# Optimization experiments

Hardware: AMD Instinct MI355X
Metric: run time of the kernel (lower is better)

Reference implementation:

```python
import jax, jax.numpy as jnp
import numpy as np

NUM_LEVELS = 16
MIN_RES = 16
MAX_RES = 4096
LOG2_HASHMAP_SIZE = 19
FEATURES_PER_LEVEL = 2
TABLE_SIZE = 1 << LOG2_HASHMAP_SIZE
HASH_INIT_SCALE = 0.001
N_POINTS = 1 << 20

_growth = np.exp((np.log(MAX_RES) - np.log(MIN_RES)) / (NUM_LEVELS - 1))
SCALINGS = jnp.asarray(np.floor(MIN_RES * _growth ** np.arange(NUM_LEVELS)), dtype=jnp.float32)  # [L]
HASH_OFFSET = jnp.arange(NUM_LEVELS, dtype=jnp.int32) * TABLE_SIZE  # [L]
PRIMES = jnp.array([1, 2654435761, 805459861], dtype=jnp.uint32)
# corner selection (1 -> ceil, 0 -> floor) matching hashed_0..hashed_7 in the torch code
CORNER_MASK = jnp.array([[1,1,1],[1,0,1],[0,0,1],[0,1,1],[1,1,0],[1,0,0],[0,0,0],[0,1,0]], dtype=bool)


def _hash(coords):
    # coords: int32 [..., L, 3]. torch uses int64 products, but since TABLE_SIZE
    # is a power of two dividing 2^32, uint32 wraparound is bit-identical mod TABLE_SIZE.
    u = coords.astype(jnp.uint32) * PRIMES
    h = u[..., 0] ^ u[..., 1] ^ u[..., 2]
    h = h & jnp.uint32(TABLE_SIZE - 1)
    return h.astype(jnp.int32) + HASH_OFFSET  # [..., L]


def setup_inputs() -> dict:
    key = jax.random.key(0)
    kx, kt = jax.random.split(key)
    x = jax.random.uniform(kx, (N_POINTS, 3), dtype=jnp.float32)
    hash_table = (jax.random.uniform(kt, (TABLE_SIZE * NUM_LEVELS, FEATURES_PER_LEVEL),
                                     dtype=jnp.float32) * 2.0 - 1.0) * HASH_INIT_SCALE
    return {"x": x, "hash_table": hash_table}


def reference(x, hash_table):
    # x: [N, 3] in [0,1]; hash_table: [TABLE_SIZE*L, F]
    scaled = x[:, None, :] * SCALINGS[None, :, None]          # [N, L, 3]
    scaled_f = jnp.floor(scaled)
    scaled_c = jnp.ceil(scaled)
    offset = scaled - scaled_f                                 # [N, L, 3]
    cf = scaled_f.astype(jnp.int32)
    cc = scaled_c.astype(jnp.int32)
    corners = jnp.where(CORNER_MASK[:, None, None, :], cc[None], cf[None])  # [8, N, L, 3]
    idx = _hash(corners)                                       # [8, N, L]
    f = hash_table[idx]                                        # [8, N, L, F]
    ox, oy, oz = offset[..., 0:1], offset[..., 1:2], offset[..., 2:3]
    f03 = f[0] * ox + f[3] * (1 - ox)
    f12 = f[1] * ox + f[2] * (1 - ox)
    f56 = f[5] * ox + f[6] * (1 - ox)
    f47 = f[4] * ox + f[7] * (1 - ox)
    f0312 = f03 * oy + f12 * (1 - oy)
    f4756 = f47 * oy + f56 * (1 - oy)
    enc = f0312 * oz + f4756 * (1 - oz)                        # [N, L, F]
    return enc.reshape(enc.shape[0], NUM_LEVELS * FEATURES_PER_LEVEL)  # [N, L*F]
```

## Files before the change

### kernel.cpp

```cpp
#include <hip/hip_runtime.h>
#include <hip/hip_fp16.h>
#include <math.h>

#define NPTS   (1u << 20)
#define NLVL   16
#define NGRID  5
#define TBITS  19
#define TMASK  ((1u << TBITS) - 1u)
#define CHUNKS (NPTS / 256u)
#define PR1    2654435761u
#define PR2    805459861u

struct Params {
    float    s[NLVL];
    uint32_t gdim[NGRID];
    uint32_t goff[NGRID];
    uint32_t vcum[NGRID + 1];
};

__device__ __forceinline__ void load_pair(const float2* __restrict__ t,
                                          uint32_t iF, uint32_t iC,
                                          float2& vF, float2& vC)
{
    const uint32_t d = iF ^ iC;
    if (d == 1u) {
        const float4 q = *(const float4*)(t + (iF & ~1u));
        if (iF & 1u) { vF = make_float2(q.z, q.w); vC = make_float2(q.x, q.y); }
        else         { vF = make_float2(q.x, q.y); vC = make_float2(q.z, q.w); }
    } else if (iC == iF + 1u || iF == iC + 1u) {
        const uint32_t lo = (iF < iC) ? iF : iC;
        const float4 q = *(const float4*)(t + lo);
        if (iF == lo) { vF = make_float2(q.x, q.y); vC = make_float2(q.z, q.w); }
        else          { vF = make_float2(q.z, q.w); vC = make_float2(q.x, q.y); }
    } else {
        vF = t[iF]; vC = t[iC];
    }
}

__device__ __forceinline__ float2 lerp8(float2 f0, float2 f1, float2 f2, float2 f3,
                                        float2 f4, float2 f5, float2 f6, float2 f7,
                                        float ox, float oy, float oz)
{
    const float omx = 1.0f - ox, omy = 1.0f - oy, omz = 1.0f - oz;
    const float a0 = f0.x * ox + f3.x * omx, b0 = f0.y * ox + f3.y * omx;
    const float a1 = f1.x * ox + f2.x * omx, b1 = f1.y * ox + f2.y * omx;
    const float a2 = f5.x * ox + f6.x * omx, b2 = f5.y * ox + f6.y * omx;
    const float a3 = f4.x * ox + f7.x * omx, b3 = f4.y * ox + f7.y * omx;
    const float c0 = a0 * oy + a1 * omy, d0 = b0 * oy + b1 * omy;
    const float c1 = a3 * oy + a2 * omy, d1 = b3 * oy + b2 * omy;
    return make_float2(c0 * oz + c1 * omz, d0 * oz + d1 * omz);
}

__device__ __forceinline__ float2 eval_hash(float x0, float x1, float x2,
                                            float s, uint32_t l,
                                            const float2* __restrict__ table)
{
    const float sx = x0 * s, sy = x1 * s, sz = x2 * s;
    const float fxf = floorf(sx), fyf = floorf(sy), fzf = floorf(sz);
    const float cxf = ceilf(sx),  cyf = ceilf(sy),  czf = ceilf(sz);
    const float ox = sx - fxf, oy = sy - fyf, oz = sz - fzf;

    const uint32_t fx = (uint32_t)fxf, cx = (uint32_t)cxf;
    const uint32_t Yf = (uint32_t)fyf * PR1,  Yc = (uint32_t)cyf * PR1;
    const uint32_t Zf = (uint32_t)fzf * PR2,  Zc = (uint32_t)czf * PR2;
    const uint32_t base = l << TBITS;

    const uint32_t i0 = ((cx ^ Yc ^ Zc) & TMASK) + base;
    const uint32_t i1 = ((cx ^ Yf ^ Zc) & TMASK) + base;
    const uint32_t i2 = ((fx ^ Yf ^ Zc) & TMASK) + base;
    const uint32_t i3 = ((fx ^ Yc ^ Zc) & TMASK) + base;
    const uint32_t i4 = ((cx ^ Yc ^ Zf) & TMASK) + base;
    const uint32_t i5 = ((cx ^ Yf ^ Zf) & TMASK) + base;
    const uint32_t i6 = ((fx ^ Yf ^ Zf) & TMASK) + base;
    const uint32_t i7 = ((fx ^ Yc ^ Zf) & TMASK) + base;

    float2 f0, f1, f2, f3, f4, f5, f6, f7;
    load_pair(table, i3, i0, f3, f0);
    load_pair(table, i2, i1, f2, f1);
    load_pair(table, i7, i4, f7, f4);
    load_pair(table, i6, i5, f6, f5);
    return lerp8(f0, f1, f2, f3, f4, f5, f6, f7, ox, oy, oz);
}

__device__ __forceinline__ float2 eval_grid(float x0, float x1, float x2,
                                            float s,
                                            const float2* __restrict__ g,
                                            uint32_t d)
{
    const float sx = x0 * s, sy = x1 * s, sz = x2 * s;
    const float fxf = floorf(sx), fyf = floorf(sy), fzf = floorf(sz);
    const float cxf = ceilf(sx),  cyf = ceilf(sy),  czf = ceilf(sz);
    const float ox = sx - fxf, oy = sy - fyf, oz = sz - fzf;

    const uint32_t fx = (uint32_t)fxf, fy = (uint32_t)fyf, fz = (uint32_t)fzf;
    const uint32_t cy = (uint32_t)cyf, cz = (uint32_t)czf;
    const bool xadj = ((uint32_t)cxf == fx + 1u);

    const uint32_t bA = (cz * d + cy) * d + fx;
    const uint32_t bB = (cz * d + fy) * d + fx;
    const uint32_t bC = (fz * d + cy) * d + fx;
    const uint32_t bD = (fz * d + fy) * d + fx;
    const float4 qA = *(const float4*)(g + bA);
    const float4 qB = *(const float4*)(g + bB);
    const float4 qC = *(const float4*)(g + bC);
    const float4 qD = *(const float4*)(g + bD);

    const float2 f3 = make_float2(qA.x, qA.y);
    const float2 f0 = xadj ? make_float2(qA.z, qA.w) : f3;
    const float2 f2 = make_float2(qB.x, qB.y);
    const float2 f1 = xadj ? make_float2(qB.z, qB.w) : f2;
    const float2 f7 = make_float2(qC.x, qC.y);
    const float2 f4 = xadj ? make_float2(qC.z, qC.w) : f7;
    const float2 f6 = make_float2(qD.x, qD.y);
    const float2 f5 = xadj ? make_float2(qD.z, qD.w) : f6;
    return lerp8(f0, f1, f2, f3, f4, f5, f6, f7, ox, oy, oz);
}

__global__ __launch_bounds__(256)
void build_grids(const float2* __restrict__ table, float2* __restrict__ gridbuf,
                 Params P)
{
    const uint32_t t = blockIdx.x * 256u + threadIdx.x;
    if (t >= P.vcum[NGRID]) return;
    uint32_t l = 0;
    #pragma unroll
    for (int i = 1; i < NGRID; ++i) if (t >= P.vcum[i]) l = i;
    const uint32_t v = t - P.vcum[l];
    const uint32_t d = P.gdim[l];
    const uint32_t vz = v / (d * d);
    const uint32_t r1 = v - vz * d * d;
    const uint32_t vy = r1 / d;
    const uint32_t vx = r1 - vy * d;
    const uint32_t h = ((vx ^ (vy * PR1) ^ (vz * PR2)) & TMASK) + (l << TBITS);
    gridbuf[P.goff[l] + v] = table[h];
}

__global__ __launch_bounds__(256)
void gather16(const float* __restrict__ x,
              const float2* __restrict__ table,
              const float2* __restrict__ gridbuf,
              __half2* __restrict__ stage,
              Params P)
{
    const uint32_t l = blockIdx.x / CHUNKS;
    const uint32_t p = (blockIdx.x % CHUNKS) * 256u + threadIdx.x;

    const float x0 = x[p * 3 + 0];
    const float x1 = x[p * 3 + 1];
    const float x2 = x[p * 3 + 2];

    float2 e;
    if (l < NGRID)
        e = eval_grid(x0, x1, x2, P.s[l], gridbuf + P.goff[l], P.gdim[l]);
    else
        e = eval_hash(x0, x1, x2, P.s[l], l, table);
    stage[l * NPTS + p] = __floats2half2_rn(e.x, e.y);
}

__global__ __launch_bounds__(256)
void transpose_kernel(const __half2* __restrict__ stage, float4* __restrict__ out4)
{
    const uint32_t e = blockIdx.x * 256u + threadIdx.x;
    const uint32_t p = e >> 3;
    const uint32_t j = e & 7u;
    const float2 a = __half22float2(stage[(2u*j)     * NPTS + p]);
    const float2 b = __half22float2(stage[(2u*j + 1) * NPTS + p]);
    out4[e] = make_float4(a.x, a.y, b.x, b.y);
}

__global__ __launch_bounds__(256)
void hashenc_fused(const float* __restrict__ x,
                   const float2* __restrict__ table,
                   float2* __restrict__ out,
                   Params P)
{
    const uint32_t tid = blockIdx.x * 256u + threadIdx.x;
    const uint32_t p = tid >> 4;
    const uint32_t l = tid & 15u;
    out[p * 16u + l] = eval_hash(x[p*3+0], x[p*3+1], x[p*3+2], P.s[l], l, table);
}

extern "C" void kernel_launch(void* const* d_in, const int* in_sizes, int n_in,
                              void* d_out, int out_size, void* d_ws, size_t ws_size,
                              hipStream_t stream) {
    const float*  x     = (const float*)d_in[0];
    const float2* table = (const float2*)d_in[1];

    Params P;
    const double growth = exp((log(4096.0) - log(16.0)) / 15.0);
    for (int l = 0; l < NLVL; ++l)
        P.s[l] = (float)floor(16.0 * pow(growth, (double)l));

    uint32_t vtot = 0;
    for (int l = 0; l < NGRID; ++l) {
        const uint32_t d = (uint32_t)P.s[l] + 1u;
        P.gdim[l] = d;
        P.vcum[l] = vtot;
        P.goff[l] = vtot;
        vtot += d * d * d;
    }
    P.vcum[NGRID] = vtot;

    const size_t grid_bytes  = (((size_t)vtot * sizeof(float2)) + 255u) & ~(size_t)255u;
    const size_t stage_bytes = (size_t)NPTS * NLVL * sizeof(__half2);
    const size_t ws_needed   = grid_bytes + stage_bytes;

    if (ws_size >= ws_needed) {
        float2*  gridbuf = (float2*)d_ws;
        __half2* stage   = (__half2*)((char*)d_ws + grid_bytes);
        float4*  out4    = (float4*)d_out;

        dim3 b256(256u);
        hipLaunchKernelGGL(build_grids, dim3((vtot + 255u) / 256u), b256, 0, stream,
                           table, gridbuf, P);
        hipLaunchKernelGGL(gather16, dim3(NLVL * CHUNKS), b256, 0, stream,
                           x, table, gridbuf, stage, P);
        hipLaunchKernelGGL(transpose_kernel, dim3(NPTS * 8u / 256u), b256, 0, stream,
                           stage, out4);
    } else {
        float2* out = (float2*)d_out;
        hipLaunchKernelGGL(hashenc_fused, dim3(NPTS * NLVL / 256u), dim3(256u), 0, stream,
                           x, table, out, P);
    }
}
```

Measured before the change: 378.7 us.

## Issue table gathers via inline asm with sc0 hint and nontemporal stage/output stores

Replaces the compiler-generated gather loads in the hash and grid evaluators with inline-asm global_load instructions carrying an sc0 cache hint. All four pair loads are issued before a single vmcnt(0) wait, so the gathers overlap. The fp16 stage writes and the final output writes become nontemporal stores to reduce cache pollution. Forcing the wait and blocking the scheduler with a sched barrier may limit compiler scheduling, and the changed cache policy could hurt reuse of the hash table.

Result: slower. 388.3 us (+2.5%).

```diff
diff --git a/kernel.cpp b/kernel.cpp
--- a/kernel.cpp
+++ b/kernel.cpp
@@ -11,6 +11,8 @@
 #define PR1    2654435761u
 #define PR2    805459861u
 
+typedef float vf4 __attribute__((ext_vector_type(4)));
+
 struct Params {
     float    s[NLVL];
     uint32_t gdim[NGRID];
@@ -18,23 +20,37 @@
     uint32_t vcum[NGRID + 1];
 };
 
-__device__ __forceinline__ void load_pair(const float2* __restrict__ t,
-                                          uint32_t iF, uint32_t iC,
-                                          float2& vF, float2& vC)
-{
-    const uint32_t d = iF ^ iC;
-    if (d == 1u) {
-        const float4 q = *(const float4*)(t + (iF & ~1u));
-        if (iF & 1u) { vF = make_float2(q.z, q.w); vC = make_float2(q.x, q.y); }
-        else         { vF = make_float2(q.x, q.y); vC = make_float2(q.z, q.w); }
-    } else if (iC == iF + 1u || iF == iC + 1u) {
-        const uint32_t lo = (iF < iC) ? iF : iC;
-        const float4 q = *(const float4*)(t + lo);
-        if (iF == lo) { vF = make_float2(q.x, q.y); vC = make_float2(q.z, q.w); }
-        else          { vF = make_float2(q.z, q.w); vC = make_float2(q.x, q.y); }
+__device__ __forceinline__ void issue_pair(const float2* __restrict__ t,
+                                           uint32_t iF, uint32_t iC,
+                                           float4& q, float2& a, float2& b,
+                                           bool& merged, bool& swp)
+{
+    const uint32_t lo = iF < iC ? iF : iC;
+    const uint32_t hi = iF < iC ? iC : iF;
+    merged = (hi - lo == 1u);
+    swp    = merged && (iF == hi);
+    if (merged) {
+        asm volatile("global_load_dwordx4 %0, %1, off sc0"
+                     : "=v"(q) : "v"(t + lo));
     } else {
-        vF = t[iF]; vC = t[iC];
-    }
+        asm volatile("global_load_dwordx2 %0, %1, off sc0"
+                     : "=v"(a) : "v"(t + iF));
+        asm volatile("global_load_dwordx2 %0, %1, off sc0"
+                     : "=v"(b) : "v"(t + iC));
+    }
+}
+
+__device__ __forceinline__ float2 sel_F(const float4& q, const float2& a,
+                                        bool merged, bool swp)
+{
+    if (merged) return swp ? make_float2(q.z, q.w) : make_float2(q.x, q.y);
+    return a;
+}
+__device__ __forceinline__ float2 sel_C(const float4& q, const float2& b,
+                                        bool merged, bool swp)
+{
+    if (merged) return swp ? make_float2(q.x, q.y) : make_float2(q.z, q.w);
+    return b;
 }
 
 __device__ __forceinline__ float2 lerp8(float2 f0, float2 f1, float2 f2, float2 f3,
@@ -74,11 +90,20 @@
     const uint32_t i6 = ((fx ^ Yf ^ Zf) & TMASK) + base;
     const uint32_t i7 = ((fx ^ Yc ^ Zf) & TMASK) + base;
 
-    float2 f0, f1, f2, f3, f4, f5, f6, f7;
-    load_pair(table, i3, i0, f3, f0);
-    load_pair(table, i2, i1, f2, f1);
-    load_pair(table, i7, i4, f7, f4);
-    load_pair(table, i6, i5, f6, f5);
+    float4 qA, qB, qC, qD;
+    float2 aA, bA, aB, bB, aC, bC, aD, bD;
+    bool mA, sA, mB, sB, mC, sC, mD, sD;
+    issue_pair(table, i3, i0, qA, aA, bA, mA, sA);
+    issue_pair(table, i2, i1, qB, aB, bB, mB, sB);
+    issue_pair(table, i7, i4, qC, aC, bC, mC, sC);
+    issue_pair(table, i6, i5, qD, aD, bD, mD, sD);
+    asm volatile("s_waitcnt vmcnt(0)" ::: "memory");
+    __builtin_amdgcn_sched_barrier(0);
+
+    const float2 f3 = sel_F(qA, aA, mA, sA), f0 = sel_C(qA, bA, mA, sA);
+    const float2 f2 = sel_F(qB, aB, mB, sB), f1 = sel_C(qB, bB, mB, sB);
+    const float2 f7 = sel_F(qC, aC, mC, sC), f4 = sel_C(qC, bC, mC, sC);
+    const float2 f6 = sel_F(qD, aD, mD, sD), f5 = sel_C(qD, bD, mD, sD);
     return lerp8(f0, f1, f2, f3, f4, f5, f6, f7, ox, oy, oz);
 }
 
@@ -100,10 +125,14 @@
     const uint32_t bB = (cz * d + fy) * d + fx;
     const uint32_t bC = (fz * d + cy) * d + fx;
     const uint32_t bD = (fz * d + fy) * d + fx;
-    const float4 qA = *(const float4*)(g + bA);
-    const float4 qB = *(const float4*)(g + bB);
-    const float4 qC = *(const float4*)(g + bC);
-    const float4 qD = *(const float4*)(g + bD);
+
+    float4 qA, qB, qC, qD;
+    asm volatile("global_load_dwordx4 %0, %1, off sc0" : "=v"(qA) : "v"(g + bA));
+    asm volatile("global_load_dwordx4 %0, %1, off sc0" : "=v"(qB) : "v"(g + bB));
+    asm volatile("global_load_dwordx4 %0, %1, off sc0" : "=v"(qC) : "v"(g + bC));
+    asm volatile("global_load_dwordx4 %0, %1, off sc0" : "=v"(qD) : "v"(g + bD));
+    asm volatile("s_waitcnt vmcnt(0)" ::: "memory");
+    __builtin_amdgcn_sched_barrier(0);
 
     const float2 f3 = make_float2(qA.x, qA.y);
     const float2 f0 = xadj ? make_float2(qA.z, qA.w) : f3;
@@ -154,18 +183,37 @@
         e = eval_grid(x0, x1, x2, P.s[l], gridbuf + P.goff[l], P.gdim[l]);
     else
         e = eval_hash(x0, x1, x2, P.s[l], l, table);
-    stage[l * NPTS + p] = __floats2half2_rn(e.x, e.y);
-}
-
-__global__ __launch_bounds__(256)
-void transpose_kernel(const __half2* __restrict__ stage, float4* __restrict__ out4)
+
+    const __half2 h = __floats2half2_rn(e.x, e.y);
+    uint32_t u; __builtin_memcpy(&u, &h, 4);
+    __builtin_nontemporal_store(u, (uint32_t*)&stage[l * NPTS + p]);
+}
+
+__global__ __launch_bounds__(256)
+void transpose_kernel(const __half2* __restrict__ stage, float* __restrict__ out)
 {
     const uint32_t e = blockIdx.x * 256u + threadIdx.x;
     const uint32_t p = e >> 3;
     const uint32_t j = e & 7u;
     const float2 a = __half22float2(stage[(2u*j)     * NPTS + p]);
     const float2 b = __half22float2(stage[(2u*j + 1) * NPTS + p]);
-    out4[e] = make_float4(a.x, a.y, b.x, b.y);
+    vf4 v; v.x = a.x; v.y = a.y; v.z = b.x; v.w = b.y;
+    __builtin_nontemporal_store(v, (vf4*)(out + (size_t)e * 4u));
+}
+
+__device__ __forceinline__ void load_pair_plain(const float2* __restrict__ t,
+                                                uint32_t iF, uint32_t iC,
+                                                float2& vF, float2& vC)
+{
+    const uint32_t lo = iF < iC ? iF : iC;
+    const uint32_t hi = iF < iC ? iC : iF;
+    if (hi - lo == 1u) {
+        const float4 q = *(const float4*)(t + lo);
+        if (iF == lo) { vF = make_float2(q.x, q.y); vC = make_float2(q.z, q.w); }
+        else          { vF = make_float2(q.z, q.w); vC = make_float2(q.x, q.y); }
+    } else {
+        vF = t[iF]; vC = t[iC];
+    }
 }
 
 __global__ __launch_bounds__(256)
@@ -177,7 +225,34 @@
     const uint32_t tid = blockIdx.x * 256u + threadIdx.x;
     const uint32_t p = tid >> 4;
     const uint32_t l = tid & 15u;
-    out[p * 16u + l] = eval_hash(x[p*3+0], x[p*3+1], x[p*3+2], P.s[l], l, table);
+
+    const float x0 = x[p*3+0], x1 = x[p*3+1], x2 = x[p*3+2];
+    const float s  = P.s[l];
+    const float sx = x0 * s, sy = x1 * s, sz = x2 * s;
+    const float fxf = floorf(sx), fyf = floorf(sy), fzf = floorf(sz);
+    const float cxf = ceilf(sx),  cyf = ceilf(sy),  czf = ceilf(sz);
+    const float ox = sx - fxf, oy = sy - fyf, oz = sz - fzf;
+
+    const uint32_t fx = (uint32_t)fxf, cx = (uint32_t)cxf;
+    const uint32_t Yf = (uint32_t)fyf * PR1,  Yc = (uint32_t)cyf * PR1;
+    const uint32_t Zf = (uint32_t)fzf * PR2,  Zc = (uint32_t)czf * PR2;
+    const uint32_t base = l << TBITS;
+
+    const uint32_t i0 = ((cx ^ Yc ^ Zc) & TMASK) + base;
+    const uint32_t i1 = ((cx ^ Yf ^ Zc) & TMASK) + base;
+    const uint32_t i2 = ((fx ^ Yf ^ Zc) & TMASK) + base;
+    const uint32_t i3 = ((fx ^ Yc ^ Zc) & TMASK) + base;
+    const uint32_t i4 = ((cx ^ Yc ^ Zf) & TMASK) + base;
+    const uint32_t i5 = ((cx ^ Yf ^ Zf) & TMASK) + base;
+    const uint32_t i6 = ((fx ^ Yf ^ Zf) & TMASK) + base;
+    const uint32_t i7 = ((fx ^ Yc ^ Zf) & TMASK) + base;
+
+    float2 f0, f1, f2, f3, f4, f5, f6, f7;
+    load_pair_plain(table, i3, i0, f3, f0);
+    load_pair_plain(table, i2, i1, f2, f1);
+    load_pair_plain(table, i7, i4, f7, f4);
+    load_pair_plain(table, i6, i5, f6, f5);
+    out[p * 16u + l] = lerp8(f0, f1, f2, f3, f4, f5, f6, f7, ox, oy, oz);
 }
 
 extern "C" void kernel_launch(void* const* d_in, const int* in_sizes, int n_in,
@@ -208,7 +283,6 @@
     if (ws_size >= ws_needed) {
         float2*  gridbuf = (float2*)d_ws;
         __half2* stage   = (__half2*)((char*)d_ws + grid_bytes);
-        float4*  out4    = (float4*)d_out;
 
         dim3 b256(256u);
         hipLaunchKernelGGL(build_grids, dim3((vtot + 255u) / 256u), b256, 0, stream,
@@ -216,7 +290,7 @@
         hipLaunchKernelGGL(gather16, dim3(NLVL * CHUNKS), b256, 0, stream,
                            x, table, gridbuf, stage, P);
         hipLaunchKernelGGL(transpose_kernel, dim3(NPTS * 8u / 256u), b256, 0, stream,
-                           stage, out4);
+                           stage, (float*)d_out);
     } else {
         float2* out = (float2*)d_out;
         hipLaunchKernelGGL(hashenc_fused, dim3(NPTS * NLVL / 256u), dim3(256u), 0, stream,
```
